# Kernel optimization log

Measured on AMD Instinct MI355X. Metric: run time of the kernel, lower is better.

Reference implementation:

```python
import jax, jax.numpy as jnp
import numpy as np


def setup_inputs() -> dict:
    key = jax.random.key(0)
    k1, k2, k3, k4 = jax.random.split(key, 4)
    N, T, D, H = 64, 512, 512, 512
    x = jax.random.normal(k1, (N, T, D), dtype=jnp.float32)
    h0 = jax.random.normal(k2, (N, H), dtype=jnp.float32)
    Wx = jax.random.normal(k3, (D, 4 * H), dtype=jnp.float32) / np.sqrt(D)
    Wh = jax.random.normal(k4, (H, 4 * H), dtype=jnp.float32) / np.sqrt(H)
    b = jnp.zeros((4 * H,), dtype=jnp.float32)
    return {"x": x, "h0": h0, "Wx": Wx, "Wh": Wh, "b": b}


def _lstm(x, h0, Wx, Wh, b):
    H = h0.shape[1]
    c0 = jnp.zeros_like(h0)
    # precompute input projection for all timesteps: (N,T,4H) -> (T,N,4H)
    xW = jnp.einsum('ntd,dk->tnk', x, Wx) + b

    def step(carry, xw_t):
        prev_h, prev_c = carry
        a = xw_t + prev_h @ Wh  # (N,4H)
        ai, af, ao, ag = jnp.split(a, 4, axis=1)
        i = jax.nn.sigmoid(ai)
        f = jax.nn.sigmoid(af)
        o = jax.nn.sigmoid(ao)
        g = jnp.tanh(ag)
        next_c = f * prev_c + i * g
        next_h = o * jnp.tanh(next_c)
        return (next_h, next_c), next_h

    _, hs = jax.lax.scan(step, (h0, c0), xW)  # hs: (T,N,H)
    return jnp.transpose(hs, (1, 0, 2))  # (N,T,H)


def reference(x, h0, Wx, Wh, b):
    return _lstm(x, h0, Wx, Wh, b)
```

## Files before the change

kernel.cpp:

```cpp
#include <hip/hip_runtime.h>
#include <math.h>

constexpr int T_ = 512;
constexpr int H_ = 512;
constexpr int V_ = 2048;
constexpr int KW_ = 512;

using short8 = __attribute__((ext_vector_type(8))) short;
using f32x4  = __attribute__((ext_vector_type(4))) float;
using u16x8  = __attribute__((ext_vector_type(8))) unsigned short;

constexpr size_t OFF_WXT = 0;
constexpr size_t OFF_WHT = 4u * 1024 * 1024;
constexpr size_t OFF_HS  = 8u * 1024 * 1024;
constexpr size_t OFF_CS  = OFF_HS + 256u * 1024;
constexpr size_t OFF_XS  = OFF_CS + 128u * 1024;

__device__ __forceinline__ void split_bf16(float x, unsigned short& hi, unsigned short& lo) {
    unsigned u  = __builtin_bit_cast(unsigned, x);
    unsigned rh = (u + 0x7fffu + ((u >> 16) & 1u)) >> 16;
    hi = (unsigned short)rh;
    float hf = __builtin_bit_cast(float, rh << 16);
    float l  = x - hf;
    unsigned ul = __builtin_bit_cast(unsigned, l);
    unsigned rl = (ul + 0x7fffu + ((ul >> 16) & 1u)) >> 16;
    lo = (unsigned short)rl;
}

__device__ __forceinline__ float sigm(float x) { return 1.0f / (1.0f + __expf(-x)); }
__device__ __forceinline__ float tanh_fast(float x) {
    float xc = fminf(fmaxf(x, -15.0f), 15.0f);
    float e = __expf(-2.0f * xc);
    return (1.0f - e) / (1.0f + e);
}

__global__ __launch_bounds__(256) void prep_wt(const float* __restrict__ W,
                                               unsigned short* __restrict__ WT_hi,
                                               unsigned short* __restrict__ WT_lo) {
    __shared__ float tile[32][33];
    const int ot = blockIdx.x;
    const int kt = blockIdx.y;
    const int lx = threadIdx.x;
    const int ly = threadIdx.y;
    #pragma unroll
    for (int i = 0; i < 4; ++i) {
        const int k = kt * 32 + ly + i * 8;
        const int o = ot * 32 + lx;
        tile[ly + i * 8][lx] = W[(size_t)k * V_ + o];
    }
    __syncthreads();
    #pragma unroll
    for (int i = 0; i < 4; ++i) {
        const int o = ot * 32 + ly + i * 8;
        const int v = ((o & 511) << 2) | (o >> 9);
        const int kk = kt * 32 + lx;
        unsigned short hi, lo;
        split_bf16(tile[lx][ly + i * 8], hi, lo);
        WT_hi[(size_t)v * KW_ + kk] = hi;
        WT_lo[(size_t)v * KW_ + kk] = lo;
    }
}

__global__ __launch_bounds__(256) void prep_h0(const float* __restrict__ h0,
                                               unsigned short* __restrict__ hs,
                                               float* __restrict__ cs) {
    const int i = blockIdx.x * 256 + threadIdx.x;
    unsigned short hi, lo;
    split_bf16(h0[i], hi, lo);
    hs[i] = hi;
    hs[32768 + i] = lo;
    cs[i] = 0.0f;
}

__global__ __launch_bounds__(256) void xsplit(const float* __restrict__ x,
                                              unsigned short* __restrict__ xs,
                                              int c0, int CT) {
    const int gtid = blockIdx.x * 256 + threadIdx.x;
    const size_t xs_lo = (size_t)CT * 32768;
    const int tot = CT * 4096;
    for (int i = gtid; i < tot; i += 65536) {
        const int r  = i >> 6;
        const int d8 = (i & 63) << 3;
        const int n = r & 63, tl = r >> 6;
        const float* xp = x + ((size_t)n * T_ + (c0 + tl)) * 512 + d8;
        const float4 va = *(const float4*)xp;
        const float4 vb = *(const float4*)(xp + 4);
        unsigned short hh[8], ll[8];
        split_bf16(va.x, hh[0], ll[0]); split_bf16(va.y, hh[1], ll[1]);
        split_bf16(va.z, hh[2], ll[2]); split_bf16(va.w, hh[3], ll[3]);
        split_bf16(vb.x, hh[4], ll[4]); split_bf16(vb.y, hh[5], ll[5]);
        split_bf16(vb.z, hh[6], ll[6]); split_bf16(vb.w, hh[7], ll[7]);
        u16x8 vh = {hh[0],hh[1],hh[2],hh[3],hh[4],hh[5],hh[6],hh[7]};
        u16x8 vl = {ll[0],ll[1],ll[2],ll[3],ll[4],ll[5],ll[6],ll[7]};
        *(u16x8*)(xs + (size_t)r * 512 + d8) = vh;
        *(u16x8*)(xs + xs_lo + (size_t)r * 512 + d8) = vl;
    }
}

__global__ __launch_bounds__(256) void xw_gemm(const unsigned short* __restrict__ xs,
                                               const unsigned short* __restrict__ wxt,
                                               const float* __restrict__ bias,
                                               float* __restrict__ xw, int CT) {
    const int tid = threadIdx.x;
    const int wid = tid >> 6, lane = tid & 63;
    const int mc = lane & 15, kb = lane >> 4;
    const int gwave = blockIdx.x * 4 + wid;
    const size_t xs_lo = (size_t)CT * 32768;

    const int tiles = CT * 128;
    for (int idx = gwave; idx < tiles; idx += 1024) {
        const int mtA = idx >> 5;
        const int ng  = idx & 31;
        const short* pa  = (const short*)xs + (size_t)(mtA * 16 + mc) * 512 + kb * 8;
        const short* pal = pa + xs_lo;
        const short* pb  = (const short*)wxt + (size_t)(ng * 64 + mc) * KW_ + kb * 8;
        f32x4 acc[4] = {};
        #pragma unroll
        for (int ks = 0; ks < 16; ++ks) {
            const short8 Ah = *(const short8*)(pa + ks * 32);
            const short8 Al = *(const short8*)(pal + ks * 32);
            #pragma unroll
            for (int n2 = 0; n2 < 4; ++n2) {
                const short8 bh = *(const short8*)(pb + (size_t)n2 * 8192 + ks * 32);
                const short8 bl = *(const short8*)(pb + 1048576 + (size_t)n2 * 8192 + ks * 32);
                acc[n2] = __builtin_amdgcn_mfma_f32_16x16x32_bf16(Ah, bh, acc[n2], 0, 0, 0);
                acc[n2] = __builtin_amdgcn_mfma_f32_16x16x32_bf16(Al, bh, acc[n2], 0, 0, 0);
                acc[n2] = __builtin_amdgcn_mfma_f32_16x16x32_bf16(Ah, bl, acc[n2], 0, 0, 0);
            }
        }
        #pragma unroll
        for (int n2 = 0; n2 < 4; ++n2) {
            const int v = ng * 64 + n2 * 16 + mc;
            const float bv = bias[((v & 3) << 9) | (v >> 2)];
            #pragma unroll
            for (int j = 0; j < 4; ++j) {
                const int r = mtA * 16 + kb * 4 + j;
                xw[(size_t)r * V_ + v] = acc[n2][j] + bv;
            }
        }
    }
}

__global__ __launch_bounds__(256) void lstm_step(const unsigned short* __restrict__ wht,
                                                 unsigned short* __restrict__ hs,
                                                 float* __restrict__ cs,
                                                 const float* __restrict__ xw,
                                                 float* __restrict__ out,
                                                 int t, int tl) {
    const int tid = threadIdx.x;
    const int wid = tid >> 6, lane = tid & 63;
    const int mc = lane & 15, kb = lane >> 4;
    const int wg = blockIdx.x;

    __shared__ float red[4][64][33];

    const short* hbase = (const short*)(hs + (size_t)(t & 1) * 65536);
    const short* whb = (const short*)wht;
    const int k0 = wid * 128;

    f32x4 acc[4][2] = {};
    #pragma unroll
    for (int ks = 0; ks < 4; ++ks) {
        const int koff = k0 + ks * 32 + kb * 8;
        short8 Bh[2], Bl[2];
        #pragma unroll
        for (int nt = 0; nt < 2; ++nt) {
            const size_t bo = (size_t)(wg * 32 + nt * 16 + mc) * KW_ + koff;
            Bh[nt] = *(const short8*)(whb + bo);
            Bl[nt] = *(const short8*)(whb + 1048576 + bo);
        }
        #pragma unroll
        for (int rt = 0; rt < 4; ++rt) {
            const size_t ao = (size_t)(rt * 16 + mc) * KW_ + koff;
            const short8 Ah = *(const short8*)(hbase + ao);
            const short8 Al = *(const short8*)(hbase + 32768 + ao);
            #pragma unroll
            for (int nt = 0; nt < 2; ++nt) {
                acc[rt][nt] = __builtin_amdgcn_mfma_f32_16x16x32_bf16(Ah, Bh[nt], acc[rt][nt], 0, 0, 0);
                acc[rt][nt] = __builtin_amdgcn_mfma_f32_16x16x32_bf16(Al, Bh[nt], acc[rt][nt], 0, 0, 0);
                acc[rt][nt] = __builtin_amdgcn_mfma_f32_16x16x32_bf16(Ah, Bl[nt], acc[rt][nt], 0, 0, 0);
            }
        }
    }
    #pragma unroll
    for (int rt = 0; rt < 4; ++rt)
        #pragma unroll
        for (int nt = 0; nt < 2; ++nt)
            #pragma unroll
            for (int j = 0; j < 4; ++j)
                red[wid][rt * 16 + kb * 4 + j][nt * 16 + mc] = acc[rt][nt][j];
    __syncthreads();

    const int r = tid >> 2, qq = tid & 3;
    const float* xwr = xw + ((size_t)tl * 64 + r) * V_ + wg * 32;
    float* cp = cs + (size_t)r * 512 + wg * 8;
    float* op = out + ((size_t)r * T_ + t) * H_ + wg * 8;
    unsigned short* hdst = hs + (size_t)((t + 1) & 1) * 65536 + (size_t)r * 512 + wg * 8;
    #pragma unroll
    for (int half = 0; half < 2; ++half) {
        const int q = qq + half * 4;
        float a[4];
        #pragma unroll
        for (int c2 = 0; c2 < 4; ++c2)
            a[c2] = red[0][r][q * 4 + c2] + red[1][r][q * 4 + c2]
                  + red[2][r][q * 4 + c2] + red[3][r][q * 4 + c2];
        const float4 xv = *(const float4*)(xwr + q * 4);
        const float iv = sigm(a[0] + xv.x);
        const float fv = sigm(a[1] + xv.y);
        const float ov = sigm(a[2] + xv.z);
        const float gv = tanh_fast(a[3] + xv.w);
        const float cc = fv * cp[q] + iv * gv;
        cp[q] = cc;
        const float hv = ov * tanh_fast(cc);
        op[q] = hv;
        unsigned short hh, hl;
        split_bf16(hv, hh, hl);
        hdst[q] = hh;
        hdst[32768 + q] = hl;
    }
}

extern "C" void kernel_launch(void* const* d_in, const int* in_sizes, int n_in,
                              void* d_out, int out_size, void* d_ws, size_t ws_size,
                              hipStream_t stream) {
    const float* x  = (const float*)d_in[0];
    const float* h0 = (const float*)d_in[1];
    const float* Wx = (const float*)d_in[2];
    const float* Wh = (const float*)d_in[3];
    const float* b  = (const float*)d_in[4];
    float* out = (float*)d_out;

    char* ws = (char*)d_ws;
    unsigned short* wxt = (unsigned short*)(ws + OFF_WXT);
    unsigned short* wht = (unsigned short*)(ws + OFF_WHT);
    unsigned short* hs  = (unsigned short*)(ws + OFF_HS);
    float* cs           = (float*)(ws + OFF_CS);
    unsigned short* xs  = (unsigned short*)(ws + OFF_XS);

    int CT = 8;
    const int cands[7] = {512, 256, 128, 64, 32, 16, 8};
    for (int i = 0; i < 7; ++i) {
        size_t need = OFF_XS + (size_t)cands[i] * (131072 + 524288);
        if (need <= ws_size) { CT = cands[i]; break; }
    }
    float* xw = (float*)(ws + OFF_XS + (size_t)CT * 131072);

    prep_wt<<<dim3(64, 16), dim3(32, 8), 0, stream>>>(Wx, wxt, wxt + (size_t)V_ * KW_);
    prep_wt<<<dim3(64, 16), dim3(32, 8), 0, stream>>>(Wh, wht, wht + (size_t)V_ * KW_);
    prep_h0<<<128, 256, 0, stream>>>(h0, hs, cs);

    for (int c0 = 0; c0 < T_; c0 += CT) {
        xsplit<<<256, 256, 0, stream>>>(x, xs, c0, CT);
        xw_gemm<<<256, 256, 0, stream>>>(xs, wxt, b, xw, CT);
        for (int tl = 0; tl < CT; ++tl) {
            lstm_step<<<64, 256, 0, stream>>>(wht, hs, cs, xw, out, c0 + tl, tl);
        }
    }
}
```

Before: 5.919 ms.

## Fuse per-timestep LSTM launches into persistent cooperative kernel with flag barrier

Replaces one lstm_step launch per timestep with a cooperative kernel that loops over all timesteps in a chunk. Blocks synchronize through a global flag barrier using atomics and fences. The Wh weight fragments stay in registers for the whole chunk, and the cell state is held in registers rather than round-tripped through global memory. This removes per-step launch overhead and the repeated weight loads, at the cost of a spin-wait barrier and higher register pressure.

```diff
diff --git a/kernel.cpp b/kernel.cpp
--- a/kernel.cpp
+++ b/kernel.cpp
@@ -10,11 +10,13 @@
 using f32x4  = __attribute__((ext_vector_type(4))) float;
 using u16x8  = __attribute__((ext_vector_type(8))) unsigned short;
 
-constexpr size_t OFF_WXT = 0;
-constexpr size_t OFF_WHT = 4u * 1024 * 1024;
-constexpr size_t OFF_HS  = 8u * 1024 * 1024;
-constexpr size_t OFF_CS  = OFF_HS + 256u * 1024;
-constexpr size_t OFF_XS  = OFF_CS + 128u * 1024;
+constexpr size_t OFF_WXT   = 0;
+constexpr size_t OFF_WHT   = 4u * 1024 * 1024;
+constexpr size_t OFF_HS    = 8u * 1024 * 1024;
+constexpr size_t OFF_CS    = OFF_HS + 256u * 1024;
+constexpr size_t OFF_FLAGS = OFF_CS + 128u * 1024;
+constexpr size_t OFF_XS    = OFF_FLAGS + 16u * 1024;
+constexpr int    NFLAGS    = 4096;
 
 __device__ __forceinline__ void split_bf16(float x, unsigned short& hi, unsigned short& lo) {
     unsigned u  = __builtin_bit_cast(unsigned, x);
@@ -63,13 +65,15 @@
 
 __global__ __launch_bounds__(256) void prep_h0(const float* __restrict__ h0,
                                                unsigned short* __restrict__ hs,
-                                               float* __restrict__ cs) {
+                                               float* __restrict__ cs,
+                                               int* __restrict__ flags) {
     const int i = blockIdx.x * 256 + threadIdx.x;
     unsigned short hi, lo;
     split_bf16(h0[i], hi, lo);
     hs[i] = hi;
     hs[32768 + i] = lo;
     cs[i] = 0.0f;
+    if (i < NFLAGS) flags[i] = 0;
 }
 
 __global__ __launch_bounds__(256) void xsplit(const float* __restrict__ x,
@@ -141,12 +145,13 @@
     }
 }
 
-__global__ __launch_bounds__(256) void lstm_step(const unsigned short* __restrict__ wht,
-                                                 unsigned short* __restrict__ hs,
-                                                 float* __restrict__ cs,
-                                                 const float* __restrict__ xw,
-                                                 float* __restrict__ out,
-                                                 int t, int tl) {
+__global__ __launch_bounds__(256) void lstm_chunk(const unsigned short* __restrict__ wht,
+                                                  unsigned short* __restrict__ hs,
+                                                  float* __restrict__ cs,
+                                                  const float* __restrict__ xw,
+                                                  float* __restrict__ out,
+                                                  int* __restrict__ flags,
+                                                  int c0, int CT) {
     const int tid = threadIdx.x;
     const int wid = tid >> 6, lane = tid & 63;
     const int mc = lane & 15, kb = lane >> 4;
@@ -154,70 +159,105 @@
 
     __shared__ float red[4][64][33];
 
-    const short* hbase = (const short*)(hs + (size_t)(t & 1) * 65536);
     const short* whb = (const short*)wht;
     const int k0 = wid * 128;
 
-    f32x4 acc[4][2] = {};
+    short8 Bh[4][2], Bl[4][2];
     #pragma unroll
     for (int ks = 0; ks < 4; ++ks) {
         const int koff = k0 + ks * 32 + kb * 8;
-        short8 Bh[2], Bl[2];
         #pragma unroll
         for (int nt = 0; nt < 2; ++nt) {
             const size_t bo = (size_t)(wg * 32 + nt * 16 + mc) * KW_ + koff;
-            Bh[nt] = *(const short8*)(whb + bo);
-            Bl[nt] = *(const short8*)(whb + 1048576 + bo);
-        }
-        #pragma unroll
-        for (int rt = 0; rt < 4; ++rt) {
-            const size_t ao = (size_t)(rt * 16 + mc) * KW_ + koff;
-            const short8 Ah = *(const short8*)(hbase + ao);
-            const short8 Al = *(const short8*)(hbase + 32768 + ao);
-            #pragma unroll
-            for (int nt = 0; nt < 2; ++nt) {
-                acc[rt][nt] = __builtin_amdgcn_mfma_f32_16x16x32_bf16(Ah, Bh[nt], acc[rt][nt], 0, 0, 0);
-                acc[rt][nt] = __builtin_amdgcn_mfma_f32_16x16x32_bf16(Al, Bh[nt], acc[rt][nt], 0, 0, 0);
-                acc[rt][nt] = __builtin_amdgcn_mfma_f32_16x16x32_bf16(Ah, Bl[nt], acc[rt][nt], 0, 0, 0);
-            }
-        }
-    }
-    #pragma unroll
-    for (int rt = 0; rt < 4; ++rt)
-        #pragma unroll
-        for (int nt = 0; nt < 2; ++nt)
-            #pragma unroll
-            for (int j = 0; j < 4; ++j)
-                red[wid][rt * 16 + kb * 4 + j][nt * 16 + mc] = acc[rt][nt][j];
-    __syncthreads();
+            Bh[ks][nt] = *(const short8*)(whb + bo);
+            Bl[ks][nt] = *(const short8*)(whb + 1048576 + bo);
+        }
+    }
 
     const int r = tid >> 2, qq = tid & 3;
-    const float* xwr = xw + ((size_t)tl * 64 + r) * V_ + wg * 32;
-    float* cp = cs + (size_t)r * 512 + wg * 8;
-    float* op = out + ((size_t)r * T_ + t) * H_ + wg * 8;
-    unsigned short* hdst = hs + (size_t)((t + 1) & 1) * 65536 + (size_t)r * 512 + wg * 8;
-    #pragma unroll
-    for (int half = 0; half < 2; ++half) {
-        const int q = qq + half * 4;
-        float a[4];
-        #pragma unroll
-        for (int c2 = 0; c2 < 4; ++c2)
-            a[c2] = red[0][r][q * 4 + c2] + red[1][r][q * 4 + c2]
-                  + red[2][r][q * 4 + c2] + red[3][r][q * 4 + c2];
-        const float4 xv = *(const float4*)(xwr + q * 4);
-        const float iv = sigm(a[0] + xv.x);
-        const float fv = sigm(a[1] + xv.y);
-        const float ov = sigm(a[2] + xv.z);
-        const float gv = tanh_fast(a[3] + xv.w);
-        const float cc = fv * cp[q] + iv * gv;
-        cp[q] = cc;
-        const float hv = ov * tanh_fast(cc);
-        op[q] = hv;
-        unsigned short hh, hl;
-        split_bf16(hv, hh, hl);
-        hdst[q] = hh;
-        hdst[32768 + q] = hl;
-    }
+    float creg[2];
+    creg[0] = cs[(size_t)r * 512 + wg * 8 + qq];
+    creg[1] = cs[(size_t)r * 512 + wg * 8 + qq + 4];
+
+    for (int tl = 0; tl < CT; ++tl) {
+        const int t = c0 + tl;
+        const short* hbase = (const short*)(hs + (size_t)(t & 1) * 65536);
+
+        f32x4 acc[4][2] = {};
+        #pragma unroll
+        for (int ks = 0; ks < 4; ++ks) {
+            const int koff = k0 + ks * 32 + kb * 8;
+            #pragma unroll
+            for (int rt = 0; rt < 4; ++rt) {
+                const size_t ao = (size_t)(rt * 16 + mc) * KW_ + koff;
+                const short8 Ah = *(const short8*)(hbase + ao);
+                const short8 Al = *(const short8*)(hbase + 32768 + ao);
+                #pragma unroll
+                for (int nt = 0; nt < 2; ++nt) {
+                    acc[rt][nt] = __builtin_amdgcn_mfma_f32_16x16x32_bf16(Ah, Bh[ks][nt], acc[rt][nt], 0, 0, 0);
+                    acc[rt][nt] = __builtin_amdgcn_mfma_f32_16x16x32_bf16(Al, Bh[ks][nt], acc[rt][nt], 0, 0, 0);
+                    acc[rt][nt] = __builtin_amdgcn_mfma_f32_16x16x32_bf16(Ah, Bl[ks][nt], acc[rt][nt], 0, 0, 0);
+                }
+            }
+        }
+        #pragma unroll
+        for (int rt = 0; rt < 4; ++rt)
+            #pragma unroll
+            for (int nt = 0; nt < 2; ++nt)
+                #pragma unroll
+                for (int j = 0; j < 4; ++j)
+                    red[wid][rt * 16 + kb * 4 + j][nt * 16 + mc] = acc[rt][nt][j];
+        __syncthreads();
+
+        {
+            const float* xwr = xw + ((size_t)tl * 64 + r) * V_ + wg * 32;
+            float* op = out + ((size_t)r * T_ + t) * H_ + wg * 8;
+            unsigned short* hdst = hs + (size_t)((t + 1) & 1) * 65536 + (size_t)r * 512 + wg * 8;
+            #pragma unroll
+            for (int half = 0; half < 2; ++half) {
+                const int q = qq + half * 4;
+                float a[4];
+                #pragma unroll
+                for (int c2 = 0; c2 < 4; ++c2)
+                    a[c2] = red[0][r][q * 4 + c2] + red[1][r][q * 4 + c2]
+                          + red[2][r][q * 4 + c2] + red[3][r][q * 4 + c2];
+                const float4 xv = *(const float4*)(xwr + q * 4);
+                const float iv = sigm(a[0] + xv.x);
+                const float fv = sigm(a[1] + xv.y);
+                const float ov = sigm(a[2] + xv.z);
+                const float gv = tanh_fast(a[3] + xv.w);
+                const float cc = fv * creg[half] + iv * gv;
+                creg[half] = cc;
+                const float hv = ov * tanh_fast(cc);
+                op[q] = hv;
+                unsigned short hh, hl;
+                split_bf16(hv, hh, hl);
+                hdst[q] = hh;
+                hdst[32768 + q] = hl;
+            }
+        }
+        __syncthreads();
+
+        __threadfence();
+        __syncthreads();
+        if (tid == 0)
+            __hip_atomic_store(&flags[wg * 32], t + 1,
+                               __ATOMIC_RELAXED, __HIP_MEMORY_SCOPE_AGENT);
+        bool mine = true;
+        do {
+            if (tid < 64) {
+                int v = __hip_atomic_load(&flags[tid * 32],
+                                          __ATOMIC_ACQUIRE, __HIP_MEMORY_SCOPE_AGENT);
+                mine = (v >= t + 1);
+                if (!mine) __builtin_amdgcn_s_sleep(2);
+            }
+        } while (!__syncthreads_and(mine));
+        __builtin_amdgcn_fence(__ATOMIC_ACQUIRE, "agent");
+        __syncthreads();
+    }
+
+    cs[(size_t)r * 512 + wg * 8 + qq]     = creg[0];
+    cs[(size_t)r * 512 + wg * 8 + qq + 4] = creg[1];
 }
 
 extern "C" void kernel_launch(void* const* d_in, const int* in_sizes, int n_in,
@@ -235,6 +275,7 @@
     unsigned short* wht = (unsigned short*)(ws + OFF_WHT);
     unsigned short* hs  = (unsigned short*)(ws + OFF_HS);
     float* cs           = (float*)(ws + OFF_CS);
+    int* flags          = (int*)(ws + OFF_FLAGS);
     unsigned short* xs  = (unsigned short*)(ws + OFF_XS);
 
     int CT = 8;
@@ -247,13 +288,15 @@
 
     prep_wt<<<dim3(64, 16), dim3(32, 8), 0, stream>>>(Wx, wxt, wxt + (size_t)V_ * KW_);
     prep_wt<<<dim3(64, 16), dim3(32, 8), 0, stream>>>(Wh, wht, wht + (size_t)V_ * KW_);
-    prep_h0<<<128, 256, 0, stream>>>(h0, hs, cs);
+    prep_h0<<<128, 256, 0, stream>>>(h0, hs, cs, flags);
 
     for (int c0 = 0; c0 < T_; c0 += CT) {
         xsplit<<<256, 256, 0, stream>>>(x, xs, c0, CT);
         xw_gemm<<<256, 256, 0, stream>>>(xs, wxt, b, xw, CT);
-        for (int tl = 0; tl < CT; ++tl) {
-            lstm_step<<<64, 256, 0, stream>>>(wht, hs, cs, xw, out, c0 + tl, tl);
-        }
-    }
-}
+        int cc0 = c0, cct = CT;
+        void* kwh = (void*)wht; void* khs = (void*)hs; void* kcs = (void*)cs;
+        void* kxw = (void*)xw; void* ko = (void*)out; void* kfl = (void*)flags;
+        void* args[] = { &kwh, &khs, &kcs, &kxw, &ko, &kfl, &cc0, &cct };
+        hipLaunchCooperativeKernel((void*)lstm_chunk, dim3(64), dim3(256), args, 0, stream);
+    }
+}
```

Measured after the change: 8.700 ms. 1.47x slower.
